# Optimization experiments

Measured on AMD Instinct MI355X. Metric: run time of the kernel, lower is better.

Reference implementation:

```python
import jax, jax.numpy as jnp
import numpy as np

NUM_LAYERS = 9
HIDDEN = 3


def _param_indices(hidden, num_layers):
    # Mirrors DistributionFreeModel.calculate_parameter_indices
    offset = 3 + (num_layers - 2) * (hidden + 2)
    idx = [((0 * hidden, 1 * hidden), (1 * hidden, 2 * hidden), (2 * hidden, 3 * hidden))]
    for o in range(3, offset, hidden + 2):
        idx.append((
            (o * hidden, (o + hidden) * hidden),
            ((o + hidden) * hidden, (o + hidden + 1) * hidden),
            ((o + hidden + 1) * hidden, (o + hidden + 2) * hidden),
        ))
    idx.append(((offset * hidden, (offset + 1) * hidden),
                ((offset + 1) * hidden, (offset + 1) * hidden + 1),
                None))
    return idx


def _cdf(inputs, parameters, hidden=HIDDEN, num_layers=NUM_LAYERS):
    # inputs: [B, F]; parameters: [F, P]
    out = inputs[..., None]  # [B, F, 1]
    for li, (wi, bi, si) in enumerate(_param_indices(hidden, num_layers)):
        w = parameters[..., wi[0]:wi[1]]
        b = parameters[..., bi[0]:bi[1]]
        if li == 0:
            w = w.reshape(w.shape[:-1] + (hidden, 1))
        elif li == num_layers - 1:
            w = w.reshape(w.shape[:-1] + (1, hidden))
        else:
            w = w.reshape(w.shape[:-1] + (hidden, hidden))
        w = jax.nn.softplus(w)
        # per-feature tiny matmul, broadcast over batch: [B,F,f] x [F,d,f] -> [B,F,d]
        out = jnp.einsum('...f,...df->...d', out, w) + b
        if si is not None:
            s = jnp.tanh(parameters[..., si[0]:si[1]])
            out = out + s * jnp.tanh(out)
    return jax.nn.sigmoid(out)[..., 0]  # squeeze last dim -> [B, F]


def setup_inputs() -> dict:
    key = jax.random.key(0)
    k1, k2 = jax.random.split(key)
    B, F = 32768, 512
    P = (NUM_LAYERS - 2) * HIDDEN ** 2 + 2 * NUM_LAYERS * HIDDEN + 1  # 118
    inputs = jax.random.normal(k1, (B, F), dtype=jnp.float32)
    parameters = jax.random.normal(k2, (F, P), dtype=jnp.float32)
    return {"inputs": inputs, "parameters": parameters}


def reference(inputs, parameters):
    return _cdf(inputs, parameters)
```

## Files before the change

### kernel.cpp

```cpp
#include <hip/hip_runtime.h>
#include <math.h>

#define NF 512
#define NP 118
#define NPPAD 126
#define FT 16
#define ROWS 8
#define BLOCK_ROWS 128
#define WS_NEED ((size_t)(NPPAD * NF) * sizeof(float))

typedef float v2f __attribute__((ext_vector_type(2)));

__device__ __forceinline__ v2f f_PP(v2f a, v2f b, v2f c) {
    v2f d; asm("v_pk_fma_f32 %0, %1, %2, %3" : "=v"(d) : "v"(a), "v"(b), "v"(c)); return d;
}
__device__ __forceinline__ v2f f_LP(v2f a, v2f b, v2f c) {
    v2f d; asm("v_pk_fma_f32 %0, %1, %2, %3 op_sel_hi:[1,0,1]" : "=v"(d) : "v"(a), "v"(b), "v"(c)); return d;
}
__device__ __forceinline__ v2f f_HP(v2f a, v2f b, v2f c) {
    v2f d; asm("v_pk_fma_f32 %0, %1, %2, %3 op_sel:[0,1,0] op_sel_hi:[1,1,1]" : "=v"(d) : "v"(a), "v"(b), "v"(c)); return d;
}
__device__ __forceinline__ v2f f_LH(v2f a, v2f b, v2f c) {
    v2f d; asm("v_pk_fma_f32 %0, %1, %2, %3 op_sel:[0,0,1] op_sel_hi:[1,0,1]" : "=v"(d) : "v"(a), "v"(b), "v"(c)); return d;
}
__device__ __forceinline__ v2f f_HL(v2f a, v2f b, v2f c) {
    v2f d; asm("v_pk_fma_f32 %0, %1, %2, %3 op_sel:[0,1,0] op_sel_hi:[1,1,0]" : "=v"(d) : "v"(a), "v"(b), "v"(c)); return d;
}

__device__ __forceinline__ float fast_rcp(float x) { return __builtin_amdgcn_rcpf(x); }

__device__ __forceinline__ float exp2_fast(float x) {
#if __has_builtin(__builtin_amdgcn_exp2f)
    return __builtin_amdgcn_exp2f(x);
#else
    return __expf(x * 0.6931471805599453f);
#endif
}

__device__ __forceinline__ float tanh1(float x) {
    float e = exp2_fast(x * 2.8853900817779268f);
    return fmaf(-2.0f, fast_rcp(e + 1.0f), 1.0f);
}
__device__ __forceinline__ v2f tanh_pair(v2f a) {
    v2f t;
    t.x = tanh1(a.x);
    t.y = tanh1(a.y);
    return t;
}
__device__ __forceinline__ float sigmoid1(float x) {
    return fast_rcp(1.0f + exp2_fast(x * -1.4426950408889634f));
}

__device__ __forceinline__ float transform_one(float v, int j) {
    int cls;
    if (j < 3) cls = 0;
    else if (j < 6) cls = 1;
    else if (j < 9) cls = 2;
    else if (j < 114) { int k = (j - 9) % 15; cls = (k < 9) ? 0 : ((k < 12) ? 1 : 2); }
    else if (j < 117) cls = 0;
    else cls = 1;
    if (cls == 0) return fmaxf(v, 0.0f) + log1pf(expf(-fabsf(v)));
    if (cls == 2) return tanhf(v);
    return v;
}

__device__ __forceinline__ bool map_padded(int jp, int* j) {
    if (jp < 9) { *j = jp; return true; }
    if (jp == 9) return false;
    if (jp < 122) {
        int k = (jp - 10) & 15, li = (jp - 10) >> 4;
        if (k == 15) return false;
        *j = 9 + 15 * li + k;
        return true;
    }
    *j = 114 + (jp - 122);
    return true;
}

__device__ __forceinline__ float transform_padded(const float* __restrict__ prow, int jp) {
    int j;
    if (!map_padded(jp, &j)) return 0.0f;
    return transform_one(prow[j], j);
}

__global__ void xform_kernel(const float* __restrict__ p, float* __restrict__ t) {
    int idx = blockIdx.x * 256 + threadIdx.x;
    if (idx < NPPAD * NF) {
        int jp = idx / NF, f = idx - jp * NF;
        t[idx] = transform_padded(p + f * NP, jp);
    }
}

template <bool FUSE_XFORM>
__global__ __launch_bounds__(256, 8)
void cdf_kernel(const float* __restrict__ x, const float* __restrict__ prm,
                float* __restrict__ out) {
    __shared__ float ldsp[NPPAD * FT];
    const int tid = threadIdx.x;
    const int fi  = tid & (FT - 1);
    const int rg  = tid >> 4;
    const int f0  = blockIdx.x * FT;
    const int b0  = blockIdx.y * BLOCK_ROWS + rg * ROWS;
    const int f   = f0 + fi;

    if constexpr (FUSE_XFORM) {
        for (int idx = tid; idx < NPPAD * FT; idx += 256) {
            int jp = idx >> 4, fl = idx & (FT - 1);
            ldsp[(jp >> 1) * (2 * FT) + fl * 2 + (jp & 1)] =
                transform_padded(prm + (f0 + fl) * NP, jp);
        }
    } else {
        for (int idx = tid; idx < NPPAD * FT; idx += 256) {
            int jp = idx >> 4, fl = idx & (FT - 1);
            ldsp[(jp >> 1) * (2 * FT) + fl * 2 + (jp & 1)] = prm[jp * NF + f0 + fl];
        }
    }

    v2f xin[4];
#pragma unroll
    for (int r = 0; r < 4; ++r) {
        xin[r].x = x[(b0 + 2 * r)     * NF + f];
        xin[r].y = x[(b0 + 2 * r + 1) * NF + f];
    }

    __syncthreads();

    const float* Pp = ldsp + fi * 2;
#define PRMV(JP) (*reinterpret_cast<const v2f*>(Pp + (JP) * FT))

    v2f h0[4], h1[4], h2[4];
    {
        v2f q0 = PRMV(0), q1 = PRMV(2), q2 = PRMV(4), q3 = PRMV(6), q4 = PRMV(8);
#pragma unroll
        for (int r = 0; r < 4; ++r) {
            v2f a0 = f_LH(xin[r], q0, q1);
            v2f a1 = f_HL(xin[r], q0, q2);
            v2f a2 = f_LH(xin[r], q1, q2);
            v2f T0 = tanh_pair(a0);
            v2f T1 = tanh_pair(a1);
            v2f T2 = tanh_pair(a2);
            h0[r] = f_LP(T0, q3, a0);
            h1[r] = f_HP(T1, q3, a1);
            h2[r] = f_LP(T2, q4, a2);
        }
    }
#pragma unroll
    for (int li = 1; li < 8; ++li) {
        const int bp = 10 + 16 * (li - 1);
        v2f q0 = PRMV(bp + 0), q1 = PRMV(bp + 2), q2 = PRMV(bp + 4), q3 = PRMV(bp + 6);
        v2f q4 = PRMV(bp + 8), q5 = PRMV(bp + 10), q6 = PRMV(bp + 12), q7 = PRMV(bp + 14);
#pragma unroll
        for (int r = 0; r < 4; ++r) {
            v2f t0 = f_LH(h0[r], q0, q4);
            t0     = f_HP(h1[r], q0, t0);
            v2f a0 = f_LP(h2[r], q1, t0);
            v2f t1 = f_HL(h0[r], q1, q5);
            t1     = f_LP(h1[r], q2, t1);
            v2f a1 = f_HP(h2[r], q2, t1);
            v2f t2 = f_LH(h0[r], q3, q5);
            t2     = f_HP(h1[r], q3, t2);
            v2f a2 = f_LP(h2[r], q4, t2);
            v2f T0 = tanh_pair(a0);
            v2f T1 = tanh_pair(a1);
            v2f T2 = tanh_pair(a2);
            h0[r] = f_LP(T0, q6, a0);
            h1[r] = f_HP(T1, q6, a1);
            h2[r] = f_LP(T2, q7, a2);
        }
    }
    {
        v2f q8 = PRMV(122), q9 = PRMV(124);
#pragma unroll
        for (int r = 0; r < 4; ++r) {
            v2f a = f_LH(h0[r], q8, q9);
            a     = f_HP(h1[r], q8, a);
            a     = f_LP(h2[r], q9, a);
            out[(b0 + 2 * r)     * NF + f] = sigmoid1(a.x);
            out[(b0 + 2 * r + 1) * NF + f] = sigmoid1(a.y);
        }
    }
#undef PRMV
}

extern "C" void kernel_launch(void* const* d_in, const int* in_sizes, int n_in,
                              void* d_out, int out_size, void* d_ws, size_t ws_size,
                              hipStream_t stream) {
    const float* x = (const float*)d_in[0];
    const float* p = (const float*)d_in[1];
    float* out = (float*)d_out;

    const int B = in_sizes[0] / NF;
    dim3 grid(NF / FT, B / BLOCK_ROWS);
    dim3 block(256);

    if (ws_size >= WS_NEED) {
        float* t = (float*)d_ws;
        xform_kernel<<<(NPPAD * NF + 255) / 256, 256, 0, stream>>>(p, t);
        cdf_kernel<false><<<grid, block, 0, stream>>>(x, t, out);
    } else {
        cdf_kernel<true><<<grid, block, 0, stream>>>(x, p, out);
    }
}
```

Measured before the change: 107.9 us.

## Replace two-thirds of tanh evaluations with LDS piecewise-linear lookup table

Builds a 2048-entry piecewise-linear tanh table (slope, intercept) covering [-8, 8] in the transform kernel and loads it into LDS. Two of the three tanh evaluations per layer now use the table, splitting the work between the transcendental unit and the LDS/VALU path; the third still uses exp2 plus rcp. The tile shape also changes (32 features by 64 rows) and the occupancy hint is dropped. The cost is 16 KB more LDS per block, which may lower occupancy, plus LDS bank conflicts from data-dependent gathers. The approximation error is larger than the exp-based tanh, and inputs are clamped outside the table range.

```diff
diff --git a/kernel.cpp b/kernel.cpp
--- a/kernel.cpp
+++ b/kernel.cpp
@@ -4,10 +4,11 @@
 #define NF 512
 #define NP 118
 #define NPPAD 126
-#define FT 16
+#define FT 32
 #define ROWS 8
-#define BLOCK_ROWS 128
-#define WS_NEED ((size_t)(NPPAD * NF) * sizeof(float))
+#define BLOCK_ROWS 64
+#define TBL_N 2048
+#define WS_NEED ((size_t)(NPPAD * NF + 2 * TBL_N) * sizeof(float))
 
 typedef float v2f __attribute__((ext_vector_type(2)));
 
@@ -28,7 +29,6 @@
 }
 
 __device__ __forceinline__ float fast_rcp(float x) { return __builtin_amdgcn_rcpf(x); }
-
 __device__ __forceinline__ float exp2_fast(float x) {
 #if __has_builtin(__builtin_amdgcn_exp2f)
     return __builtin_amdgcn_exp2f(x);
@@ -37,18 +37,28 @@
 #endif
 }
 
-__device__ __forceinline__ float tanh1(float x) {
+__device__ __forceinline__ float tanh_exp1(float x) {
     float e = exp2_fast(x * 2.8853900817779268f);
     return fmaf(-2.0f, fast_rcp(e + 1.0f), 1.0f);
 }
-__device__ __forceinline__ v2f tanh_pair(v2f a) {
-    v2f t;
-    t.x = tanh1(a.x);
-    t.y = tanh1(a.y);
-    return t;
+__device__ __forceinline__ v2f tanh_exp_pair(v2f a) {
+    v2f t; t.x = tanh_exp1(a.x); t.y = tanh_exp1(a.y); return t;
 }
 __device__ __forceinline__ float sigmoid1(float x) {
     return fast_rcp(1.0f + exp2_fast(x * -1.4426950408889634f));
+}
+
+__device__ __forceinline__ v2f tanh_lut_pair(v2f a, const v2f* __restrict__ tbl,
+                                             v2f K128, v2f KIdx) {
+    v2f xi = f_PP(a, K128, KIdx);
+    unsigned i0 = (unsigned)__builtin_amdgcn_fmed3f(xi.x, 0.0f, (float)(TBL_N - 1));
+    unsigned i1 = (unsigned)__builtin_amdgcn_fmed3f(xi.y, 0.0f, (float)(TBL_N - 1));
+    v2f g0 = tbl[i0];
+    v2f g1 = tbl[i1];
+    v2f t;
+    t.x = fmaf(a.x, g0.x, g0.y);
+    t.y = fmaf(a.y, g1.x, g1.y);
+    return t;
 }
 
 __device__ __forceinline__ float transform_one(float v, int j) {
@@ -83,37 +93,62 @@
     return transform_one(prow[j], j);
 }
 
+__device__ __forceinline__ void tbl_entry(int b, float* s, float* c) {
+    float xl = (float)b * (1.0f / 128.0f) - (1024.5f / 128.0f);
+    float xr = xl + (1.0f / 128.0f);
+    float t0 = tanhf(xl), t1 = tanhf(xr);
+    float sl = (t1 - t0) * 128.0f;
+    *s = sl;
+    *c = fmaf(-sl, xl, t0);
+}
+
 __global__ void xform_kernel(const float* __restrict__ p, float* __restrict__ t) {
     int idx = blockIdx.x * 256 + threadIdx.x;
     if (idx < NPPAD * NF) {
         int jp = idx / NF, f = idx - jp * NF;
         t[idx] = transform_padded(p + f * NP, jp);
+    } else if (idx < NPPAD * NF + TBL_N) {
+        int bin = idx - NPPAD * NF;
+        float s, c;
+        tbl_entry(bin, &s, &c);
+        t[NPPAD * NF + 2 * bin]     = s;
+        t[NPPAD * NF + 2 * bin + 1] = c;
     }
 }
 
 template <bool FUSE_XFORM>
-__global__ __launch_bounds__(256, 8)
+__global__ __launch_bounds__(256)
 void cdf_kernel(const float* __restrict__ x, const float* __restrict__ prm,
                 float* __restrict__ out) {
     __shared__ float ldsp[NPPAD * FT];
+    __shared__ v2f   tblv[TBL_N];
     const int tid = threadIdx.x;
     const int fi  = tid & (FT - 1);
-    const int rg  = tid >> 4;
+    const int rg  = tid >> 5;
     const int f0  = blockIdx.x * FT;
     const int b0  = blockIdx.y * BLOCK_ROWS + rg * ROWS;
     const int f   = f0 + fi;
 
     if constexpr (FUSE_XFORM) {
         for (int idx = tid; idx < NPPAD * FT; idx += 256) {
-            int jp = idx >> 4, fl = idx & (FT - 1);
+            int jp = idx >> 5, fl = idx & (FT - 1);
             ldsp[(jp >> 1) * (2 * FT) + fl * 2 + (jp & 1)] =
                 transform_padded(prm + (f0 + fl) * NP, jp);
         }
+        float* tf = (float*)tblv;
+        for (int bin = tid; bin < TBL_N; bin += 256) {
+            float s, c; tbl_entry(bin, &s, &c);
+            tf[2 * bin] = s; tf[2 * bin + 1] = c;
+        }
     } else {
         for (int idx = tid; idx < NPPAD * FT; idx += 256) {
-            int jp = idx >> 4, fl = idx & (FT - 1);
+            int jp = idx >> 5, fl = idx & (FT - 1);
             ldsp[(jp >> 1) * (2 * FT) + fl * 2 + (jp & 1)] = prm[jp * NF + f0 + fl];
         }
+        float* tf = (float*)tblv;
+        const float* tw = prm + NPPAD * NF;
+        for (int idx = tid; idx < 2 * TBL_N; idx += 256)
+            tf[idx] = tw[idx];
     }
 
     v2f xin[4];
@@ -124,6 +159,9 @@
     }
 
     __syncthreads();
+
+    const v2f K128 = {128.0f, 128.0f};
+    const v2f KIdx = {1024.5f, 1024.5f};
 
     const float* Pp = ldsp + fi * 2;
 #define PRMV(JP) (*reinterpret_cast<const v2f*>(Pp + (JP) * FT))
@@ -136,9 +174,9 @@
             v2f a0 = f_LH(xin[r], q0, q1);
             v2f a1 = f_HL(xin[r], q0, q2);
             v2f a2 = f_LH(xin[r], q1, q2);
-            v2f T0 = tanh_pair(a0);
-            v2f T1 = tanh_pair(a1);
-            v2f T2 = tanh_pair(a2);
+            v2f T0 = tanh_lut_pair(a0, tblv, K128, KIdx);
+            v2f T1 = tanh_lut_pair(a1, tblv, K128, KIdx);
+            v2f T2 = tanh_exp_pair(a2);
             h0[r] = f_LP(T0, q3, a0);
             h1[r] = f_HP(T1, q3, a1);
             h2[r] = f_LP(T2, q4, a2);
@@ -160,9 +198,9 @@
             v2f t2 = f_LH(h0[r], q3, q5);
             t2     = f_HP(h1[r], q3, t2);
             v2f a2 = f_LP(h2[r], q4, t2);
-            v2f T0 = tanh_pair(a0);
-            v2f T1 = tanh_pair(a1);
-            v2f T2 = tanh_pair(a2);
+            v2f T0 = tanh_lut_pair(a0, tblv, K128, KIdx);
+            v2f T1 = tanh_lut_pair(a1, tblv, K128, KIdx);
+            v2f T2 = tanh_exp_pair(a2);
             h0[r] = f_LP(T0, q6, a0);
             h1[r] = f_HP(T1, q6, a1);
             h2[r] = f_LP(T2, q7, a2);
@@ -195,7 +233,8 @@
 
     if (ws_size >= WS_NEED) {
         float* t = (float*)d_ws;
-        xform_kernel<<<(NPPAD * NF + 255) / 256, 256, 0, stream>>>(p, t);
+        int total = NPPAD * NF + TBL_N;
+        xform_kernel<<<(total + 255) / 256, 256, 0, stream>>>(p, t);
         cdf_kernel<false><<<grid, block, 0, stream>>>(x, t, out);
     } else {
         cdf_kernel<true><<<grid, block, 0, stream>>>(x, p, out);
```

Measured after the change: 111.2 us. 1.03x slower.
